# Kernel optimization log

Hardware: AMD Instinct MI355X
Metric: run time of the kernel (lower is better)

The kernel has to match this reference:

```python
import jax, jax.numpy as jnp
import numpy as np

H = 12      # num_attention_heads
DM = 768    # hidden_size
HD = DM // H  # head_dim = 64


def setup_inputs() -> dict:
    key = jax.random.key(0)
    ks = jax.random.split(key, 9)
    B, L = 4, 2048
    s = 0.02
    return {
        "hidden_states": jax.random.normal(ks[0], (B, L, DM), jnp.float32),
        "wq": jax.random.normal(ks[1], (DM, DM), jnp.float32) * s,
        "bq": jnp.zeros((DM,), jnp.float32),
        "wk": jax.random.normal(ks[2], (DM, DM), jnp.float32) * s,
        "bk": jnp.zeros((DM,), jnp.float32),
        "wv": jax.random.normal(ks[3], (DM, DM), jnp.float32) * s,
        "bv": jnp.zeros((DM,), jnp.float32),
        "wo": jax.random.normal(ks[4], (DM, DM), jnp.float32) * s,
        "bo": jnp.zeros((DM,), jnp.float32),
    }


def reference(hidden_states, wq, bq, wk, bk, wv, bv, wo, bo):
    B, L, D = hidden_states.shape
    scale = HD ** -0.5
    # torch Linear: x @ W.T + b
    q = hidden_states @ wq.T + bq
    k = hidden_states @ wk.T + bk
    v = hidden_states @ wv.T + bv
    # [B, H, L, HD]
    q = q.reshape(B, L, H, HD).transpose(0, 2, 1, 3)
    k = k.reshape(B, L, H, HD).transpose(0, 2, 1, 3)
    v = v.reshape(B, L, H, HD).transpose(0, 2, 1, 3)
    attn = jnp.einsum('bhqd,bhkd->bhqk', q, k) * scale
    causal = jnp.tril(jnp.ones((L, L), dtype=bool))
    attn = jnp.where(causal, attn, jnp.float32(-jnp.inf))
    attn = jax.nn.softmax(attn, axis=-1)
    out = jnp.einsum('bhqk,bhkd->bhqd', attn, v)
    out = out.transpose(0, 2, 1, 3).reshape(B, L, D)
    return out @ wo.T + bo
```

## Files before the change

kernel.cpp:

```cpp
#include <hip/hip_runtime.h>

typedef unsigned short ushort_t;
typedef __attribute__((ext_vector_type(8))) short short8;
typedef __attribute__((ext_vector_type(4))) float f32x4;

__device__ __forceinline__ ushort_t f2b(float f) {
    union { float f; unsigned int i; } v; v.f = f;
    unsigned int x = v.i;
    return (ushort_t)((x + 0x7fffu + ((x >> 16) & 1u)) >> 16);
}
__device__ __forceinline__ ushort_t f2b_fast(float f) {
    union { float f; unsigned int i; } v; v.f = f;
    return (ushort_t)((v.i + 0x8000u) >> 16);
}
__device__ __forceinline__ float exp2_hw(float x) {
    return __builtin_amdgcn_exp2f(x);
}
__device__ __forceinline__ void dma16(const ushort_t* g, ushort_t* l) {
    __builtin_amdgcn_global_load_lds(
        (const __attribute__((address_space(1))) unsigned int*)g,
        (__attribute__((address_space(3))) unsigned int*)l, 16, 0, 0);
}

__global__ __launch_bounds__(256)
void convert_bf16(const float* __restrict__ hs, const float* __restrict__ wq,
                  const float* __restrict__ wk, const float* __restrict__ wv,
                  const float* __restrict__ wo,
                  ushort_t* __restrict__ hsb, ushort_t* __restrict__ wqb,
                  ushort_t* __restrict__ wkb, ushort_t* __restrict__ wvb,
                  ushort_t* __restrict__ wob)
{
    const int y = blockIdx.y;
    const float* src; ushort_t* dst; int n;
    if (y == 0)      { src = hs; dst = hsb; n = 8192 * 768; }
    else if (y == 1) { src = wq; dst = wqb; n = 768 * 768; }
    else if (y == 2) { src = wk; dst = wkb; n = 768 * 768; }
    else if (y == 3) { src = wv; dst = wvb; n = 768 * 768; }
    else             { src = wo; dst = wob; n = 768 * 768; }
    const int idx = (blockIdx.x * 256 + threadIdx.x) * 8;
    if (idx >= n) return;
    const float4 a = ((const float4*)(src + idx))[0];
    const float4 b = ((const float4*)(src + idx))[1];
    ushort_t tmp[8] = { f2b(a.x), f2b(a.y), f2b(a.z), f2b(a.w),
                        f2b(b.x), f2b(b.y), f2b(b.z), f2b(b.w) };
    *(uint4*)(dst + idx) = *(const uint4*)tmp;
}

#define NIT 12

template<int MODE>
__global__ __launch_bounds__(256, 2)
void gemm_mfma(const ushort_t* __restrict__ A,
               const ushort_t* __restrict__ W0, const ushort_t* __restrict__ W1,
               const ushort_t* __restrict__ W2,
               const float* __restrict__ b0, const float* __restrict__ b1,
               const float* __restrict__ b2,
               void* __restrict__ C0, void* __restrict__ C1, void* __restrict__ C2)
{
    __shared__ __attribute__((aligned(16))) ushort_t Ab[2][128 * 64];
    __shared__ __attribute__((aligned(16))) ushort_t Wb[2][128 * 64];

    const int id   = blockIdx.x;
    const int xcd  = id & 7;
    const int slot = id >> 3;
    int mtile, otile, z;
    if (MODE == 0) {
        mtile = (slot / 18) * 8 + xcd;
        const int rem = slot % 18;
        otile = rem % 6;
        z     = rem / 6;
    } else {
        mtile = (slot / 6) * 8 + xcd;
        otile = slot % 6;
        z     = 0;
    }
    const ushort_t* W = (z == 0) ? W0 : (z == 1) ? W1 : W2;
    const float* bias  = (z == 0) ? b0 : (z == 1) ? b1 : b2;
    void* C            = (z == 0) ? C0 : (z == 1) ? C1 : C2;

    const int t    = threadIdx.x;
    const int lane = t & 63;
    const int w    = t >> 6;
    const int col  = lane & 15;
    const int kg   = lane >> 4;
    const int m0   = mtile * 128;
    const int o0   = otile * 128;
    const int mh   = (w & 1) * 64;
    const int oh   = (w >> 1) * 64;

    f32x4 acc[4][4];
#pragma unroll
    for (int mt = 0; mt < 4; ++mt)
#pragma unroll
        for (int nt = 0; nt < 4; ++nt) acc[mt][nt] = (f32x4){0.f, 0.f, 0.f, 0.f};

    const int lrow = lane >> 3;
    const int lgr  = (lane & 7) ^ lrow;
    const ushort_t* pa = A + (size_t)(m0 + lrow) * 768 + lgr * 8;
    const ushort_t* pw = W + (size_t)(o0 + lrow) * 768 + lgr * 8;

    float bias_v[4];
#pragma unroll
    for (int nt = 0; nt < 4; ++nt) bias_v[nt] = bias[o0 + oh + nt * 16 + col];

    auto stage = [&](int c, int b) {
#pragma unroll
        for (int j = 0; j < 4; ++j) {
            const int q = 4 * w + j;
            dma16(pa + (size_t)q * (8 * 768) + c * 64, &Ab[b][q * 512]);
            dma16(pw + (size_t)q * (8 * 768) + c * 64, &Wb[b][q * 512]);
        }
    };

    stage(0, 0);

    const int c7   = col & 7;
    const int g0   = (kg ^ c7) * 8;
    const int g1   = ((4 + kg) ^ c7) * 8;

#pragma unroll 2
    for (int it = 0; it < NIT; ++it) {
        const int cur = it & 1;
        asm volatile("s_waitcnt vmcnt(0)" ::: "memory");
        __builtin_amdgcn_s_barrier();
        if (it + 1 < NIT) stage(it + 1, cur ^ 1);

        short8 wf[4][2], af[4][2];
#pragma unroll
        for (int nt = 0; nt < 4; ++nt) {
            const int r = (oh + nt * 16 + col) * 64;
            wf[nt][0] = *(const short8*)&Wb[cur][r + g0];
            wf[nt][1] = *(const short8*)&Wb[cur][r + g1];
        }
#pragma unroll
        for (int mt = 0; mt < 4; ++mt) {
            const int r = (mh + mt * 16 + col) * 64;
            af[mt][0] = *(const short8*)&Ab[cur][r + g0];
            af[mt][1] = *(const short8*)&Ab[cur][r + g1];
        }

#pragma unroll
        for (int mt = 0; mt < 4; ++mt)
#pragma unroll
            for (int nt = 0; nt < 4; ++nt) {
                acc[mt][nt] = __builtin_amdgcn_mfma_f32_16x16x32_bf16(
                    af[mt][0], wf[nt][0], acc[mt][nt], 0, 0, 0);
                acc[mt][nt] = __builtin_amdgcn_mfma_f32_16x16x32_bf16(
                    af[mt][1], wf[nt][1], acc[mt][nt], 0, 0, 0);
            }
    }

    const float scale = (MODE == 0 && z == 0) ? 0.18033688011112042f : 1.0f;

#pragma unroll
    for (int mt = 0; mt < 4; ++mt)
#pragma unroll
        for (int nt = 0; nt < 4; ++nt) {
            const int mb = m0 + mh + mt * 16 + kg * 4;
            const int o  = o0 + oh + nt * 16 + col;
            if (MODE == 0 && z == 2) {
                ushort_t tmp[4];
#pragma unroll
                for (int r = 0; r < 4; ++r) tmp[r] = f2b(acc[mt][nt][r] + bias_v[nt]);
                const size_t dst = ((size_t)((mb >> 11) * 12 + (o >> 6)) << 17)
                                 + ((size_t)(o & 63) << 11) + (mb & 2047);
                *(uint2*)((ushort_t*)C + dst) = *(const uint2*)tmp;
            } else {
#pragma unroll
                for (int r = 0; r < 4; ++r) {
                    const int m = mb + r;
                    const float v = (acc[mt][nt][r] + bias_v[nt]) * scale;
                    if (MODE == 0) {
                        const size_t dst = ((size_t)((m >> 11) * 12 + (o >> 6)) << 17)
                                         + ((size_t)(m & 2047) << 6) + (o & 63);
                        ((ushort_t*)C)[dst] = f2b(v);
                    } else {
                        ((float*)C)[(size_t)m * 768 + o] = v;
                    }
                }
            }
        }
}

#define KV_STRIDE 72
#define PS_STRIDE 76

__global__ __launch_bounds__(256, 3)
void attn_mfma(const ushort_t* __restrict__ Q, const ushort_t* __restrict__ K,
               const ushort_t* __restrict__ Vt, ushort_t* __restrict__ AO)
{
    __shared__ ushort_t Ks[2][64 * KV_STRIDE];
    __shared__ ushort_t Vs[2][64 * KV_STRIDE];
    __shared__ ushort_t Ps[4][16 * PS_STRIDE];

    const int t    = threadIdx.x;
    const int lane = t & 63;
    const int w    = t >> 6;
    const int id   = blockIdx.x;
    const int bh   = ((id >> 3) >> 4) * 8 + (id & 7);
    const int p    = (id >> 3) & 15;
    const size_t base = (size_t)bh << 17;

    const int col = lane & 15;
    const int kg  = lane >> 4;
    const int srow = t >> 2;
    const int scol = (t & 3) << 4;
    const int b = bh / 12, h = bh % 12;

#pragma unroll
    for (int phase = 0; phase < 2; ++phase) {
        const int tile = phase ? p : (31 - p);
        const int q0   = tile << 6;
        const int nch  = tile + 1;

        const ushort_t* pq = Q + base + (size_t)(q0 + 16 * w + col) * 64 + kg * 8;
        const short8 aq0 = *(const short8*)pq;
        const short8 aq1 = *(const short8*)(pq + 32);

        float l_lane[4] = {0.f, 0.f, 0.f, 0.f};
        f32x4 o_acc[4];
#pragma unroll
        for (int vt = 0; vt < 4; ++vt) o_acc[vt] = (f32x4){0.f, 0.f, 0.f, 0.f};

        {
            const ushort_t* pk = K  + base + (size_t)srow * 64 + scol;
            const ushort_t* pv = Vt + base + ((size_t)srow << 11) + scol;
            const uint4 ka = *(const uint4*)pk, kb = *(const uint4*)(pk + 8);
            const uint4 va = *(const uint4*)pv, vb = *(const uint4*)(pv + 8);
            *(uint4*)&Ks[0][srow * KV_STRIDE + scol]     = ka;
            *(uint4*)&Ks[0][srow * KV_STRIDE + scol + 8] = kb;
            *(uint4*)&Vs[0][srow * KV_STRIDE + scol]     = va;
            *(uint4*)&Vs[0][srow * KV_STRIDE + scol + 8] = vb;
        }
        __syncthreads();

        for (int c = 0; c < nch; ++c) {
            const int cur = c & 1;

            uint4 ka, kb, va, vb;
            if (c + 1 < nch) {
                const int k1 = (c + 1) << 6;
                const ushort_t* pk = K  + base + (size_t)(k1 + srow) * 64 + scol;
                const ushort_t* pv = Vt + base + ((size_t)srow << 11) + k1 + scol;
                ka = *(const uint4*)pk; kb = *(const uint4*)(pk + 8);
                va = *(const uint4*)pv; vb = *(const uint4*)(pv + 8);
            }

            f32x4 s[4];
            __builtin_amdgcn_s_setprio(1);
#pragma unroll
            for (int kt = 0; kt < 4; ++kt) {
                const ushort_t* pkf = &Ks[cur][(kt * 16 + col) * KV_STRIDE + kg * 8];
                const short8 b0 = *(const short8*)pkf;
                const short8 b1 = *(const short8*)(pkf + 32);
                f32x4 acc = (f32x4){0.f, 0.f, 0.f, 0.f};
                acc = __builtin_amdgcn_mfma_f32_16x16x32_bf16(aq0, b0, acc, 0, 0, 0);
                acc = __builtin_amdgcn_mfma_f32_16x16x32_bf16(aq1, b1, acc, 0, 0, 0);
                s[kt] = acc;
            }
            __builtin_amdgcn_s_setprio(0);

            const int qrow = q0 + 16 * w + 4 * kg;
            if (c == nch - 1) {
                const int k0 = c << 6;
#pragma unroll
                for (int kt = 0; kt < 4; ++kt)
#pragma unroll
                    for (int r = 0; r < 4; ++r) {
                        const int key = k0 + kt * 16 + col;
                        s[kt][r] = (key > qrow + r) ? 0.f : exp2_hw(s[kt][r]);
                    }
            } else {
#pragma unroll
                for (int kt = 0; kt < 4; ++kt)
#pragma unroll
                    for (int r = 0; r < 4; ++r) s[kt][r] = exp2_hw(s[kt][r]);
            }
#pragma unroll
            for (int r = 0; r < 4; ++r)
                l_lane[r] += (s[0][r] + s[1][r]) + (s[2][r] + s[3][r]);

            ushort_t* ps = Ps[w];
#pragma unroll
            for (int kt = 0; kt < 4; ++kt)
#pragma unroll
                for (int r = 0; r < 4; ++r)
                    ps[(4 * kg + r) * PS_STRIDE + kt * 16 + col] = f2b_fast(s[kt][r]);
            short8 pa0, pa1;
            {
                const ushort_t* pp = ps + (size_t)col * PS_STRIDE + kg * 8;
                pa0 = *(const short8*)pp;
                pa1 = *(const short8*)(pp + 32);
            }

            __builtin_amdgcn_s_setprio(1);
#pragma unroll
            for (int vt = 0; vt < 4; ++vt) {
                const ushort_t* pvf = &Vs[cur][(vt * 16 + col) * KV_STRIDE + kg * 8];
                const short8 v0 = *(const short8*)pvf;
                const short8 v1 = *(const short8*)(pvf + 32);
                f32x4 o = o_acc[vt];
                o = __builtin_amdgcn_mfma_f32_16x16x32_bf16(pa0, v0, o, 0, 0, 0);
                o = __builtin_amdgcn_mfma_f32_16x16x32_bf16(pa1, v1, o, 0, 0, 0);
                o_acc[vt] = o;
            }
            __builtin_amdgcn_s_setprio(0);

            if (c + 1 < nch) {
                const int nxt = cur ^ 1;
                *(uint4*)&Ks[nxt][srow * KV_STRIDE + scol]     = ka;
                *(uint4*)&Ks[nxt][srow * KV_STRIDE + scol + 8] = kb;
                *(uint4*)&Vs[nxt][srow * KV_STRIDE + scol]     = va;
                *(uint4*)&Vs[nxt][srow * KV_STRIDE + scol + 8] = vb;
            }
            __syncthreads();
        }

        float linv[4];
#pragma unroll
        for (int r = 0; r < 4; ++r) {
            float ls = l_lane[r];
            ls += __shfl_xor(ls, 1);
            ls += __shfl_xor(ls, 2);
            ls += __shfl_xor(ls, 4);
            ls += __shfl_xor(ls, 8);
            linv[r] = 1.f / ls;
        }
#pragma unroll
        for (int vt = 0; vt < 4; ++vt)
#pragma unroll
            for (int r = 0; r < 4; ++r) {
                const int q = q0 + 16 * w + 4 * kg + r;
                AO[((size_t)(b * 2048 + q)) * 768 + h * 64 + vt * 16 + col] =
                    f2b_fast(o_acc[vt][r] * linv[r]);
            }
    }
}

extern "C" void kernel_launch(void* const* d_in, const int* in_sizes, int n_in,
                              void* d_out, int out_size, void* d_ws, size_t ws_size,
                              hipStream_t stream) {
    const float* hs = (const float*)d_in[0];
    const float* wq = (const float*)d_in[1];
    const float* bq = (const float*)d_in[2];
    const float* wk = (const float*)d_in[3];
    const float* bk = (const float*)d_in[4];
    const float* wv = (const float*)d_in[5];
    const float* bv = (const float*)d_in[6];
    const float* wo = (const float*)d_in[7];
    const float* bo = (const float*)d_in[8];
    float* out = (float*)d_out;

    const size_t NB = (size_t)8192 * 768;
    const size_t WN = (size_t)768 * 768;
    ushort_t* hsb = (ushort_t*)d_ws;
    ushort_t* Qb  = hsb + NB;
    ushort_t* Kb  = Qb + NB;
    ushort_t* Vtb = Kb + NB;
    ushort_t* wqb = Vtb + NB;
    ushort_t* wkb = wqb + WN;
    ushort_t* wvb = wkb + WN;
    ushort_t* wob = wvb + WN;
    ushort_t* AO  = hsb;

    dim3 blk(256);
    convert_bf16<<<dim3(3072, 5), blk, 0, stream>>>(hs, wq, wk, wv, wo,
                                                    hsb, wqb, wkb, wvb, wob);
    gemm_mfma<0><<<dim3(1152), blk, 0, stream>>>(hsb, wqb, wkb, wvb,
                                                 bq, bk, bv, Qb, Kb, Vtb);
    attn_mfma<<<dim3(768), blk, 0, stream>>>(Qb, Kb, Vtb, AO);
    gemm_mfma<1><<<dim3(384), blk, 0, stream>>>(AO, wob, wob, wob,
                                                bo, bo, bo, out, out, out);
}
```

Baseline: 228.9 us.

## Software-pipeline attention loop: defer PV MFMA of previous chunk behind next QK

Measured after the change: 230.8 us. About the same (+0.8%).

```diff
diff --git a/kernel.cpp b/kernel.cpp
--- a/kernel.cpp
+++ b/kernel.cpp
@@ -189,9 +189,9 @@
 void attn_mfma(const ushort_t* __restrict__ Q, const ushort_t* __restrict__ K,
                const ushort_t* __restrict__ Vt, ushort_t* __restrict__ AO)
 {
-    __shared__ ushort_t Ks[2][64 * KV_STRIDE];
+    __shared__ ushort_t Ks[64 * KV_STRIDE];
     __shared__ ushort_t Vs[2][64 * KV_STRIDE];
-    __shared__ ushort_t Ps[4][16 * PS_STRIDE];
+    __shared__ ushort_t Ps[4][2][16 * PS_STRIDE];
 
     const int t    = threadIdx.x;
     const int lane = t & 63;
@@ -222,20 +222,22 @@
 #pragma unroll
         for (int vt = 0; vt < 4; ++vt) o_acc[vt] = (f32x4){0.f, 0.f, 0.f, 0.f};
 
+        __syncthreads();
+
         {
             const ushort_t* pk = K  + base + (size_t)srow * 64 + scol;
             const ushort_t* pv = Vt + base + ((size_t)srow << 11) + scol;
             const uint4 ka = *(const uint4*)pk, kb = *(const uint4*)(pk + 8);
             const uint4 va = *(const uint4*)pv, vb = *(const uint4*)(pv + 8);
-            *(uint4*)&Ks[0][srow * KV_STRIDE + scol]     = ka;
-            *(uint4*)&Ks[0][srow * KV_STRIDE + scol + 8] = kb;
+            *(uint4*)&Ks[srow * KV_STRIDE + scol]        = ka;
+            *(uint4*)&Ks[srow * KV_STRIDE + scol + 8]    = kb;
             *(uint4*)&Vs[0][srow * KV_STRIDE + scol]     = va;
             *(uint4*)&Vs[0][srow * KV_STRIDE + scol + 8] = vb;
         }
-        __syncthreads();
 
         for (int c = 0; c < nch; ++c) {
-            const int cur = c & 1;
+            const int cur = c & 1, prv = cur ^ 1;
+            __syncthreads();
 
             uint4 ka, kb, va, vb;
             if (c + 1 < nch) {
@@ -246,11 +248,32 @@
                 va = *(const uint4*)pv; vb = *(const uint4*)(pv + 8);
             }
 
+            if (c > 0) {
+                short8 pa0, pa1;
+                {
+                    const ushort_t* pp = Ps[w][prv] + (size_t)col * PS_STRIDE + kg * 8;
+                    pa0 = *(const short8*)pp;
+                    pa1 = *(const short8*)(pp + 32);
+                }
+                __builtin_amdgcn_s_setprio(1);
+#pragma unroll
+                for (int vt = 0; vt < 4; ++vt) {
+                    const ushort_t* pvf = &Vs[prv][(vt * 16 + col) * KV_STRIDE + kg * 8];
+                    const short8 v0 = *(const short8*)pvf;
+                    const short8 v1 = *(const short8*)(pvf + 32);
+                    f32x4 o = o_acc[vt];
+                    o = __builtin_amdgcn_mfma_f32_16x16x32_bf16(pa0, v0, o, 0, 0, 0);
+                    o = __builtin_amdgcn_mfma_f32_16x16x32_bf16(pa1, v1, o, 0, 0, 0);
+                    o_acc[vt] = o;
+                }
+                __builtin_amdgcn_s_setprio(0);
+            }
+
             f32x4 s[4];
             __builtin_amdgcn_s_setprio(1);
 #pragma unroll
             for (int kt = 0; kt < 4; ++kt) {
-                const ushort_t* pkf = &Ks[cur][(kt * 16 + col) * KV_STRIDE + kg * 8];
+                const ushort_t* pkf = &Ks[(kt * 16 + col) * KV_STRIDE + kg * 8];
                 const short8 b0 = *(const short8*)pkf;
                 const short8 b1 = *(const short8*)(pkf + 32);
                 f32x4 acc = (f32x4){0.f, 0.f, 0.f, 0.f};
@@ -280,23 +303,36 @@
             for (int r = 0; r < 4; ++r)
                 l_lane[r] += (s[0][r] + s[1][r]) + (s[2][r] + s[3][r]);
 
-            ushort_t* ps = Ps[w];
-#pragma unroll
-            for (int kt = 0; kt < 4; ++kt)
-#pragma unroll
-                for (int r = 0; r < 4; ++r)
-                    ps[(4 * kg + r) * PS_STRIDE + kt * 16 + col] = f2b_fast(s[kt][r]);
+            {
+                ushort_t* ps = Ps[w][cur];
+#pragma unroll
+                for (int kt = 0; kt < 4; ++kt)
+#pragma unroll
+                    for (int r = 0; r < 4; ++r)
+                        ps[(4 * kg + r) * PS_STRIDE + kt * 16 + col] = f2b_fast(s[kt][r]);
+            }
+
+            if (c + 1 < nch) {
+                __syncthreads();
+                *(uint4*)&Ks[srow * KV_STRIDE + scol]          = ka;
+                *(uint4*)&Ks[srow * KV_STRIDE + scol + 8]      = kb;
+                *(uint4*)&Vs[prv][srow * KV_STRIDE + scol]     = va;
+                *(uint4*)&Vs[prv][srow * KV_STRIDE + scol + 8] = vb;
+            }
+        }
+
+        {
+            const int pb = (nch - 1) & 1;
             short8 pa0, pa1;
             {
-                const ushort_t* pp = ps + (size_t)col * PS_STRIDE + kg * 8;
+                const ushort_t* pp = Ps[w][pb] + (size_t)col * PS_STRIDE + kg * 8;
                 pa0 = *(const short8*)pp;
                 pa1 = *(const short8*)(pp + 32);
             }
-
             __builtin_amdgcn_s_setprio(1);
 #pragma unroll
             for (int vt = 0; vt < 4; ++vt) {
-                const ushort_t* pvf = &Vs[cur][(vt * 16 + col) * KV_STRIDE + kg * 8];
+                const ushort_t* pvf = &Vs[pb][(vt * 16 + col) * KV_STRIDE + kg * 8];
                 const short8 v0 = *(const short8*)pvf;
                 const short8 v1 = *(const short8*)(pvf + 32);
                 f32x4 o = o_acc[vt];
@@ -305,15 +341,6 @@
                 o_acc[vt] = o;
             }
             __builtin_amdgcn_s_setprio(0);
-
-            if (c + 1 < nch) {
-                const int nxt = cur ^ 1;
-                *(uint4*)&Ks[nxt][srow * KV_STRIDE + scol]     = ka;
-                *(uint4*)&Ks[nxt][srow * KV_STRIDE + scol + 8] = kb;
-                *(uint4*)&Vs[nxt][srow * KV_STRIDE + scol]     = va;
-                *(uint4*)&Vs[nxt][srow * KV_STRIDE + scol + 8] = vb;
-            }
-            __syncthreads();
         }
 
         float linv[4];
```
